# Optimization experiments

Measured on AMD Instinct MI355X. Metric: run time of the kernel, lower is better.

The kernel has to match this reference:

```python
import jax, jax.numpy as jnp
import numpy as np

HID = 64
NUM_LAYERS = 2
EPS = 1e-5


def _layernorm(x, g, b):
    mu = jnp.mean(x, axis=-1, keepdims=True)
    var = jnp.mean(jnp.square(x - mu), axis=-1, keepdims=True)
    return (x - mu) * jax.lax.rsqrt(var + EPS) * g + b


def _mlp(x, w1, b1, g, beta, w2, b2):
    # Linear -> LayerNorm -> ReLU -> Linear (torch Linear: x @ W.T + b)
    h = x @ w1.T + b1
    h = jax.nn.relu(_layernorm(h, g, beta))
    return h @ w2.T + b2


def _gru(x, h, wih, whh, bih, bhh):
    # PyTorch GRUCell semantics
    gi = x @ wih.T + bih
    gh = h @ whh.T + bhh
    ir, iz, inn = jnp.split(gi, 3, axis=-1)
    hr, hz, hn = jnp.split(gh, 3, axis=-1)
    r = jax.nn.sigmoid(ir + hr)
    z = jax.nn.sigmoid(iz + hz)
    n = jnp.tanh(inn + r * hn)
    return (1.0 - z) * n + z * h


def setup_inputs() -> dict:
    key = jax.random.key(0)
    ks = iter(jax.random.split(key, 64))
    s = 0.05

    def rn(shape):
        return jax.random.normal(next(ks), shape, dtype=jnp.float32) * s

    B, M, K1 = 32, 256, 128
    inp = {
        'hybrid_input': jax.random.normal(next(ks), (B, M, K1, 4), dtype=jnp.float32),
        'hidden_state': jnp.zeros((B, HID), dtype=jnp.float32),
        # input encoder
        'enc_w1': rn((HID, 4)), 'enc_b1': rn((HID,)),
        'enc_g': jnp.ones((HID,), jnp.float32), 'enc_beta': jnp.zeros((HID,), jnp.float32),
        'enc_w2': rn((HID, HID)), 'enc_b2': rn((HID,)),
        # per-layer, per-side (axis0=layer, axis1=[row,col]) params
        'l_w1': rn((NUM_LAYERS, 2, HID, HID)), 'l_b1': rn((NUM_LAYERS, 2, HID)),
        'l_g': jnp.ones((NUM_LAYERS, 2, HID), jnp.float32), 'l_beta': jnp.zeros((NUM_LAYERS, 2, HID), jnp.float32),
        'l_w2': rn((NUM_LAYERS, 2, HID, HID)), 'l_b2': rn((NUM_LAYERS, 2, HID)),
        'l_gwih': rn((NUM_LAYERS, 2, 3 * HID, HID)), 'l_gwhh': rn((NUM_LAYERS, 2, 3 * HID, HID)),
        'l_gbih': rn((NUM_LAYERS, 2, 3 * HID)), 'l_gbhh': rn((NUM_LAYERS, 2, 3 * HID)),
        # top-level GRU
        'g_wih': rn((3 * HID, HID)), 'g_whh': rn((3 * HID, HID)),
        'g_bih': rn((3 * HID,)), 'g_bhh': rn((3 * HID,)),
        # head: Linear(2H->H) -> ReLU -> Linear(H->1)
        'head_w1': rn((HID, 2 * HID)), 'head_b1': rn((HID,)),
        'head_w2': rn((1, HID)), 'head_b2': rn((1,)),
    }
    return inp


def reference(hybrid_input, hidden_state, enc_w1, enc_b1, enc_g, enc_beta, enc_w2, enc_b2,
              l_w1, l_b1, l_g, l_beta, l_w2, l_b2, l_gwih, l_gwhh, l_gbih, l_gbhh,
              g_wih, g_whh, g_bih, g_bhh, head_w1, head_b1, head_w2, head_b2):
    # input encoder
    x = _mlp(hybrid_input, enc_w1, enc_b1, enc_g, enc_beta, enc_w2, enc_b2)

    for l in range(NUM_LAYERS):
        # row pass: max over axis 2 (K+1)
        row_max = jnp.max(x, axis=2, keepdims=True)
        upd = _mlp(x - row_max, l_w1[l, 0], l_b1[l, 0], l_g[l, 0], l_beta[l, 0], l_w2[l, 0], l_b2[l, 0])
        x = _gru(upd, x, l_gwih[l, 0], l_gwhh[l, 0], l_gbih[l, 0], l_gbhh[l, 0])
        # col pass: max over axis 1 (M)
        col_max = jnp.max(x, axis=1, keepdims=True)
        upd = _mlp(x - col_max, l_w1[l, 1], l_b1[l, 1], l_g[l, 1], l_beta[l, 1], l_w2[l, 1], l_b2[l, 1])
        x = _gru(upd, x, l_gwih[l, 1], l_gwhh[l, 1], l_gbih[l, 1], l_gbhh[l, 1])

    B, M, K1, h = x.shape
    global_feat = jnp.max(x.reshape(B, M * K1, h), axis=1)  # (B, H)
    new_hidden = _gru(global_feat, hidden_state, g_wih, g_whh, g_bih, g_bhh)

    h_exp = jnp.broadcast_to(new_hidden[:, None, None, :], (B, M, K1, h))
    combined = jnp.concatenate([x, h_exp], axis=-1)  # (B, M, K1, 2H)
    hh = jax.nn.relu(combined @ head_w1.T + head_b1)
    logits = (hh @ head_w2.T + head_b2)[..., 0]  # (B, M, K1)
    return logits, new_hidden
```

## Files before the change

kernel.cpp:

```cpp
#include <hip/hip_runtime.h>
#include <math.h>

typedef unsigned int u32;
typedef unsigned short u16;
typedef __attribute__((ext_vector_type(4))) float f32x4;
typedef __attribute__((ext_vector_type(8))) short s16x8;

#define NTOT 1048576
#define SWZ(n, col) ((col) ^ (((n) & 7) << 4))

__device__ __forceinline__ u16 f2bf(float f) {
  u32 u = __float_as_uint(f);
  u32 r = ((u >> 16) & 1u) + 0x7fffu;
  return (u16)((u + r) >> 16);
}
__device__ __forceinline__ float bflo(u32 v) { return __uint_as_float(v << 16); }
__device__ __forceinline__ float bfhi(u32 v) { return __uint_as_float(v & 0xffff0000u); }
__device__ __forceinline__ u32 pk2(float a, float b) {
  return (u32)f2bf(a) | ((u32)f2bf(b) << 16);
}
__device__ __forceinline__ float sigm(float x) {
  return __builtin_amdgcn_rcpf(1.0f + __expf(-x));
}
__device__ __forceinline__ float tanh_f(float x) {
  float e = __expf(2.0f * x);
  return 1.0f - 2.0f * __builtin_amdgcn_rcpf(e + 1.0f);
}
__device__ __forceinline__ float relu(float x) { return fmaxf(x, 0.0f); }

__device__ __forceinline__ void gemm16(const unsigned char* L, int aoff, int boff,
                                       int w, int lq, int lr, f32x4 acc[4]) {
  const int l = lq * 16 + lr;
  s16x8 a0 = *(const s16x8*)(L + aoff + ((w * 2 + 0) * 64 + l) * 16);
  s16x8 a1 = *(const s16x8*)(L + aoff + ((w * 2 + 1) * 64 + l) * 16);
  const int c0 = ((lq << 4)) ^ ((lr & 7) << 4);
  const unsigned char* Bp = L + boff + lr * 128;
#pragma unroll
  for (int nt = 0; nt < 4; ++nt) {
    s16x8 b0 = *(const s16x8*)(Bp + nt * 2048 + c0);
    s16x8 b1 = *(const s16x8*)(Bp + nt * 2048 + (c0 ^ 64));
    acc[nt] = __builtin_amdgcn_mfma_f32_16x16x32_bf16(a0, b0, acc[nt], 0, 0, 0);
    acc[nt] = __builtin_amdgcn_mfma_f32_16x16x32_bf16(a1, b1, acc[nt], 0, 0, 0);
  }
}

__device__ __forceinline__ void binit(f32x4 acc[4], float x, float y, float z, float w) {
  f32x4 v; v[0] = x; v[1] = y; v[2] = z; v[3] = w;
#pragma unroll
  for (int nt = 0; nt < 4; ++nt) acc[nt] = v;
}

__global__ void diag_kernel(float* out, float v) { out[0] = v; }

__global__ __launch_bounds__(256) void prep_kernel(
    const float* __restrict__ enc_w2, const float* __restrict__ head_w1,
    const float* __restrict__ l_w1, const float* __restrict__ l_w2,
    const float* __restrict__ l_gwih, const float* __restrict__ l_gwhh,
    ushort* __restrict__ gwF) {
  const int id = blockIdx.x;
  const int t = threadIdx.x;
  const float* src;
  int ld = 64;
  if (id == 0)      { src = enc_w2; }
  else if (id == 1) { src = head_w1; ld = 128; }
  else if (id < 6)  { src = l_w1 + (id - 2) * 4096; }
  else if (id < 10) { src = l_w2 + (id - 6) * 4096; }
  else if (id < 22) { int q = id - 10; src = l_gwih + (q / 3) * 12288 + (q % 3) * 4096; }
  else              { int q = id - 22; src = l_gwhh + (q / 3) * 12288 + (q % 3) * 4096; }
  uint4* dst = (uint4*)(gwF + (size_t)id * 4096);
#pragma unroll
  for (int i = 0; i < 2; ++i) {
    int ch = i * 256 + t;
    int q = ch & 63;
    int g = ch >> 6;
    int j = (g >> 1) * 16 + (q & 15);
    int k = (g & 1) * 32 + (q >> 4) * 8;
    const float* s = src + (size_t)j * ld + k;
    float4 f0 = *(const float4*)(s);
    float4 f1 = *(const float4*)(s + 4);
    uint4 o;
    o.x = pk2(f0.x, f0.y); o.y = pk2(f0.z, f0.w);
    o.z = pk2(f1.x, f1.y); o.w = pk2(f1.z, f1.w);
    dst[ch] = o;
  }
}

__global__ __launch_bounds__(256) void encoder_kernel(
    const float4* __restrict__ hyb, ushort* __restrict__ xG,
    const ushort* __restrict__ gwF, const float* __restrict__ enc_w1,
    const float* __restrict__ b1, const float* __restrict__ gg,
    const float* __restrict__ be, const float* __restrict__ b2) {
  __shared__ __align__(16) unsigned char L[25600];
  const int t = threadIdx.x;
  const int w = t >> 6, l = t & 63, lq = l >> 4, lr = l & 15;
  const int gbase = blockIdx.x * 64;

  { const uint4* src = (const uint4*)gwF;
    *(uint4*)(L + 16384 + t * 16) = src[t];
    *(uint4*)(L + 16384 + (256 + t) * 16) = src[256 + t]; }
  ((float*)(L + 24576))[t] = enc_w1[t];
  __syncthreads();

  {
    const int n = t >> 2, part = t & 3;
    float4 iv = hyb[gbase + n];
    const float* W1 = (const float*)(L + 24576);
    float h[16];
#pragma unroll
    for (int jj = 0; jj < 16; ++jj) {
      int j = part * 16 + jj;
      float4 wr = *(const float4*)(W1 + j * 4);
      h[jj] = b1[j] + wr.x * iv.x + wr.y * iv.y + wr.z * iv.z + wr.w * iv.w;
    }
    float s = 0.f, q = 0.f;
#pragma unroll
    for (int jj = 0; jj < 16; ++jj) { s += h[jj]; q += h[jj] * h[jj]; }
    s += __shfl_xor(s, 1); q += __shfl_xor(q, 1);
    s += __shfl_xor(s, 2); q += __shfl_xor(q, 2);
    float mean = s * (1.f / 64.f);
    float rstd = rsqrtf(q * (1.f / 64.f) - mean * mean + 1e-5f);
    u32 pk[8];
#pragma unroll
    for (int jj = 0; jj < 16; jj += 2) {
      int j = part * 16 + jj;
      float v0 = relu((h[jj] - mean) * rstd * gg[j] + be[j]);
      float v1 = relu((h[jj + 1] - mean) * rstd * gg[j + 1] + be[j + 1]);
      pk[jj >> 1] = pk2(v0, v1);
    }
    *(uint4*)(L + n * 128 + SWZ(n, part * 32))      = make_uint4(pk[0], pk[1], pk[2], pk[3]);
    *(uint4*)(L + n * 128 + SWZ(n, part * 32 + 16)) = make_uint4(pk[4], pk[5], pk[6], pk[7]);
  }
  __syncthreads();

  const int j0 = w * 16 + lq * 4;
  float4 vb2 = *(const float4*)(b2 + j0);
  f32x4 acc[4];
  binit(acc, vb2.x, vb2.y, vb2.z, vb2.w);
  gemm16(L, 16384, 0, w, lq, lr, acc);
  const int colb = w * 32 + lq * 8;
#pragma unroll
  for (int nt = 0; nt < 4; ++nt) {
    int n = nt * 16 + lr;
    *(uint2*)(L + 8192 + n * 128 + SWZ(n, colb)) =
        make_uint2(pk2(acc[nt][0], acc[nt][1]), pk2(acc[nt][2], acc[nt][3]));
  }
  __syncthreads();
#pragma unroll
  for (int i = 0; i < 2; ++i) {
    int flat = i * 256 + t; int n = flat >> 3, c = flat & 7;
    uint4 v = *(const uint4*)(L + 8192 + n * 128 + SWZ(n, c * 16));
    ((uint4*)(xG + (size_t)gbase * 64))[(size_t)n * 8 + c] = v;
  }
}

#define LXL 0
#define LP  8192
#define LWB(i) (16384 + (i) * 8192)
#define LRED 49152

__global__ __launch_bounds__(256, 3) void pass_kernel(
    ushort* __restrict__ xG, const ushort* __restrict__ gwF,
    const float* __restrict__ rmG, const float* __restrict__ cmG, int mode,
    int s_w1, int s_w2, int s_ih0, int s_hh0,
    const float* __restrict__ b1, const float* __restrict__ b2,
    const float* __restrict__ gg, const float* __restrict__ be,
    const float* __restrict__ bih, const float* __restrict__ bhh) {
  __shared__ __align__(16) unsigned char L[51200];
  const int t = threadIdx.x;
  const int w = t >> 6, l = t & 63, lq = l >> 4, lr = l & 15;
  const int gbase = blockIdx.x * 64;
  const int j0 = w * 16 + lq * 4;
  const int colb = w * 32 + lq * 8;

  float4 vb1 = *(const float4*)(b1 + j0);
  float4 vg  = *(const float4*)(gg + j0);
  float4 vbe = *(const float4*)(be + j0);
  float4 vb2 = *(const float4*)(b2 + j0);
  float4 bi0 = *(const float4*)(bih + j0),       bh0 = *(const float4*)(bhh + j0);
  float4 bi1 = *(const float4*)(bih + 64 + j0),  bh1 = *(const float4*)(bhh + 64 + j0);
  float4 bi2 = *(const float4*)(bih + 128 + j0), bh2 = *(const float4*)(bhh + 128 + j0);

  {
    int sl[4] = {s_w1, s_w2, s_ih0, s_hh0};
#pragma unroll
    for (int sbi = 0; sbi < 4; ++sbi) {
      const uint4* src = (const uint4*)(gwF + (size_t)sl[sbi] * 4096);
      *(uint4*)(L + LWB(sbi) + t * 16) = src[t];
      *(uint4*)(L + LWB(sbi) + (256 + t) * 16) = src[256 + t];
    }
  }
  {
    const int rbase = (gbase >> 7) * 64;
    const int cbase = (gbase >> 15) * 128 + (gbase & 127);
    const uint4* xrow = (const uint4*)(xG + (size_t)gbase * 64);
#pragma unroll
    for (int i = 0; i < 2; ++i) {
      int flat = i * 256 + t; int n = flat >> 3, c = flat & 7;
      uint4 xv = xrow[(size_t)n * 8 + c];
      *(uint4*)(L + LXL + n * 128 + SWZ(n, c * 16)) = xv;
      const float* mvp = (mode == 0) ? (rmG + rbase + c * 8)
                                     : (cmG + (size_t)(cbase + n) * 64 + c * 8);
      float4 ma = *(const float4*)(mvp);
      float4 mb = *(const float4*)(mvp + 4);
      uint4 o;
      o.x = pk2(bflo(xv.x) - ma.x, bfhi(xv.x) - ma.y);
      o.y = pk2(bflo(xv.y) - ma.z, bfhi(xv.y) - ma.w);
      o.z = pk2(bflo(xv.z) - mb.x, bfhi(xv.z) - mb.y);
      o.w = pk2(bflo(xv.w) - mb.z, bfhi(xv.w) - mb.w);
      *(uint4*)(L + LP + n * 128 + SWZ(n, c * 16)) = o;
    }
  }
  __syncthreads();

  f32x4 acc[4];
  binit(acc, vb1.x, vb1.y, vb1.z, vb1.w);
  gemm16(L, LWB(0), LP, w, lq, lr, acc);
#pragma unroll
  for (int nt = 0; nt < 4; ++nt) {
    float s = acc[nt][0] + acc[nt][1] + acc[nt][2] + acc[nt][3];
    float q = acc[nt][0] * acc[nt][0] + acc[nt][1] * acc[nt][1] +
              acc[nt][2] * acc[nt][2] + acc[nt][3] * acc[nt][3];
    s += __shfl_xor(s, 16); q += __shfl_xor(q, 16);
    s += __shfl_xor(s, 32); q += __shfl_xor(q, 32);
    if (lq == 0) *(float2*)(L + LRED + (w * 64 + nt * 16 + lr) * 8) = make_float2(s, q);
  }
  __syncthreads();
  {
    const uint4* src = (const uint4*)(gwF + (size_t)(s_ih0 + 1) * 4096);
    *(uint4*)(L + LWB(0) + t * 16) = src[t];
    *(uint4*)(L + LWB(0) + (256 + t) * 16) = src[256 + t];
  }
  {
    float gv[4] = {vg.x, vg.y, vg.z, vg.w};
    float bv[4] = {vbe.x, vbe.y, vbe.z, vbe.w};
#pragma unroll
    for (int nt = 0; nt < 4; ++nt) {
      int n = nt * 16 + lr;
      float ss = 0.f, qq = 0.f;
#pragma unroll
      for (int wv = 0; wv < 4; ++wv) {
        float2 pr = *(const float2*)(L + LRED + (wv * 64 + n) * 8);
        ss += pr.x; qq += pr.y;
      }
      float mean = ss * (1.f / 64.f);
      float rstd = rsqrtf(qq * (1.f / 64.f) - mean * mean + 1e-5f);
      float h_[4];
#pragma unroll
      for (int r = 0; r < 4; ++r) h_[r] = relu((acc[nt][r] - mean) * rstd * gv[r] + bv[r]);
      *(uint2*)(L + LP + n * 128 + SWZ(n, colb)) =
          make_uint2(pk2(h_[0], h_[1]), pk2(h_[2], h_[3]));
    }
  }
  __syncthreads();

  binit(acc, vb2.x, vb2.y, vb2.z, vb2.w);
  gemm16(L, LWB(1), LP, w, lq, lr, acc);
  __syncthreads();
  {
    const uint4* src = (const uint4*)(gwF + (size_t)(s_hh0 + 1) * 4096);
    *(uint4*)(L + LWB(1) + t * 16) = src[t];
    *(uint4*)(L + LWB(1) + (256 + t) * 16) = src[256 + t];
  }
#pragma unroll
  for (int nt = 0; nt < 4; ++nt) {
    int n = nt * 16 + lr;
    *(uint2*)(L + LP + n * 128 + SWZ(n, colb)) =
        make_uint2(pk2(acc[nt][0], acc[nt][1]), pk2(acc[nt][2], acc[nt][3]));
  }
  __syncthreads();

  binit(acc, bi0.x + bh0.x, bi0.y + bh0.y, bi0.z + bh0.z, bi0.w + bh0.w);
  gemm16(L, LWB(2), LP, w, lq, lr, acc);
  gemm16(L, LWB(3), LXL, w, lq, lr, acc);
  float rg[4][4];
#pragma unroll
  for (int nt = 0; nt < 4; ++nt)
#pragma unroll
    for (int r = 0; r < 4; ++r) rg[nt][r] = sigm(acc[nt][r]);
  __syncthreads();
  {
    const uint4* s2 = (const uint4*)(gwF + (size_t)(s_ih0 + 2) * 4096);
    const uint4* s3 = (const uint4*)(gwF + (size_t)(s_hh0 + 2) * 4096);
    *(uint4*)(L + LWB(2) + t * 16) = s2[t];
    *(uint4*)(L + LWB(2) + (256 + t) * 16) = s2[256 + t];
    *(uint4*)(L + LWB(3) + t * 16) = s3[t];
    *(uint4*)(L + LWB(3) + (256 + t) * 16) = s3[256 + t];
  }
  binit(acc, bi1.x + bh1.x, bi1.y + bh1.y, bi1.z + bh1.z, bi1.w + bh1.w);
  gemm16(L, LWB(0), LP, w, lq, lr, acc);
  gemm16(L, LWB(1), LXL, w, lq, lr, acc);
  float zg[4][4];
#pragma unroll
  for (int nt = 0; nt < 4; ++nt)
#pragma unroll
    for (int r = 0; r < 4; ++r) zg[nt][r] = sigm(acc[nt][r]);
  __syncthreads();

  f32x4 ai[4], ah[4];
  binit(ai, bi2.x, bi2.y, bi2.z, bi2.w);
  gemm16(L, LWB(2), LP, w, lq, lr, ai);
  binit(ah, bh2.x, bh2.y, bh2.z, bh2.w);
  gemm16(L, LWB(3), LXL, w, lq, lr, ah);

  float xn[4][4];
#pragma unroll
  for (int nt = 0; nt < 4; ++nt) {
    int n = nt * 16 + lr;
    uint2 xo = *(const uint2*)(L + LXL + n * 128 + SWZ(n, colb));
    float xv[4] = {bflo(xo.x), bfhi(xo.x), bflo(xo.y), bfhi(xo.y)};
#pragma unroll
    for (int r = 0; r < 4; ++r) {
      float nn = tanh_f(ai[nt][r] + rg[nt][r] * ah[nt][r]);
      xn[nt][r] = (1.0f - zg[nt][r]) * nn + zg[nt][r] * xv[r];
    }
  }
  __syncthreads();
#pragma unroll
  for (int nt = 0; nt < 4; ++nt) {
    int n = nt * 16 + lr;
    *(uint2*)(L + LXL + n * 128 + SWZ(n, colb)) =
        make_uint2(pk2(xn[nt][0], xn[nt][1]), pk2(xn[nt][2], xn[nt][3]));
  }
  __syncthreads();
#pragma unroll
  for (int i = 0; i < 2; ++i) {
    int flat = i * 256 + t; int n = flat >> 3, c = flat & 7;
    uint4 v = *(const uint4*)(L + LXL + n * 128 + SWZ(n, c * 16));
    ((uint4*)(xG + (size_t)gbase * 64))[(size_t)n * 8 + c] = v;
  }
}

__global__ __launch_bounds__(256) void rowmax_kernel(const ushort* __restrict__ xG,
                                                     float* __restrict__ rm) {
  __shared__ float red[8][64];
  const int t = threadIdx.x;
  const int col = t & 31, rg = t >> 5;
  const u32* xu = (const u32*)xG + (size_t)blockIdx.x * 128 * 32;
  float m0 = -INFINITY, m1 = -INFINITY;
#pragma unroll 4
  for (int i = 0; i < 16; ++i) {
    u32 v = xu[(size_t)(rg + i * 8) * 32 + col];
    m0 = fmaxf(m0, bflo(v)); m1 = fmaxf(m1, bfhi(v));
  }
  red[rg][col * 2] = m0; red[rg][col * 2 + 1] = m1;
  __syncthreads();
  if (t < 64) {
    float m = red[0][t];
#pragma unroll
    for (int i = 1; i < 8; ++i) m = fmaxf(m, red[i][t]);
    rm[(size_t)blockIdx.x * 64 + t] = m;
  }
}

__global__ __launch_bounds__(256) void colmax_kernel(const ushort* __restrict__ xG,
                                                     float* __restrict__ cm) {
  const int t = threadIdx.x;
  const int b = blockIdx.x >> 4, kg = blockIdx.x & 15;
  const int col = t & 31, k1 = kg * 8 + (t >> 5);
  const u32* xu = (const u32*)xG;
  float m0 = -INFINITY, m1 = -INFINITY;
  for (int m = 0; m < 256; ++m) {
    size_t node = ((size_t)(b * 256 + m)) * 128 + k1;
    u32 v = xu[node * 32 + col];
    m0 = fmaxf(m0, bflo(v)); m1 = fmaxf(m1, bfhi(v));
  }
  float* dst = cm + ((size_t)(b * 128 + k1)) * 64 + col * 2;
  dst[0] = m0; dst[1] = m1;
}

__global__ __launch_bounds__(256) void gmax_kernel(const ushort* __restrict__ xG,
                                                   float* __restrict__ gp) {
  __shared__ float red[8][64];
  const int t = threadIdx.x;
  const int b = blockIdx.x >> 3, ng = blockIdx.x & 7;
  const int col = t & 31, rg = t >> 5;
  const u32* xu = (const u32*)xG + ((size_t)(b * 32768 + ng * 4096)) * 32;
  float m0 = -INFINITY, m1 = -INFINITY;
  for (int i = 0; i < 512; ++i) {
    u32 v = xu[(size_t)(rg + i * 8) * 32 + col];
    m0 = fmaxf(m0, bflo(v)); m1 = fmaxf(m1, bfhi(v));
  }
  red[rg][col * 2] = m0; red[rg][col * 2 + 1] = m1;
  __syncthreads();
  if (t < 64) {
    float m = red[0][t];
#pragma unroll
    for (int i = 1; i < 8; ++i) m = fmaxf(m, red[i][t]);
    gp[(size_t)blockIdx.x * 64 + t] = m;
  }
}

__global__ __launch_bounds__(64) void topgru_kernel(
    const float* __restrict__ gp, const float* __restrict__ hs,
    const float* __restrict__ gwih, const float* __restrict__ gwhh,
    const float* __restrict__ gbih, const float* __restrict__ gbhh,
    float* __restrict__ nh, float* __restrict__ outTail) {
  __shared__ float gf[64], h0[64];
  const int b = blockIdx.x, j = threadIdx.x;
  float gv = gp[b * 512 + j];
#pragma unroll
  for (int i = 1; i < 8; ++i) gv = fmaxf(gv, gp[b * 512 + i * 64 + j]);
  gf[j] = gv;
  h0[j] = hs[b * 64 + j];
  __syncthreads();
  float gi[3], gh[3];
#pragma unroll
  for (int g = 0; g < 3; ++g) {
    float s = gbih[g * 64 + j];
    const float* wr = gwih + (g * 64 + j) * 64;
    for (int k = 0; k < 64; ++k) s += wr[k] * gf[k];
    gi[g] = s;
  }
#pragma unroll
  for (int g = 0; g < 3; ++g) {
    float s = gbhh[g * 64 + j];
    const float* wr = gwhh + (g * 64 + j) * 64;
    for (int k = 0; k < 64; ++k) s += wr[k] * h0[k];
    gh[g] = s;
  }
  float rr = sigm(gi[0] + gh[0]);
  float zz = sigm(gi[1] + gh[1]);
  float nn = tanh_f(gi[2] + rr * gh[2]);
  float val = (1.0f - zz) * nn + zz * h0[j];
  nh[b * 64 + j] = val;
  outTail[b * 64 + j] = val;
}

__global__ __launch_bounds__(64) void hc_kernel(const float* __restrict__ nh,
                                                const float* __restrict__ hw1,
                                                const float* __restrict__ hb1,
                                                float* __restrict__ hc) {
  __shared__ float h0[64];
  const int b = blockIdx.x, j = threadIdx.x;
  h0[j] = nh[b * 64 + j];
  __syncthreads();
  float s = hb1[j];
  const float* wr = hw1 + j * 128 + 64;
  for (int k = 0; k < 64; ++k) s += wr[k] * h0[k];
  hc[b * 64 + j] = s;
}

__global__ __launch_bounds__(256) void head_kernel(
    const ushort* __restrict__ xG, const ushort* __restrict__ gwF,
    const float* __restrict__ hc, const float* __restrict__ hw2,
    const float* __restrict__ hb2, float* __restrict__ out) {
  __shared__ __align__(16) unsigned char L[17408];
  const int t = threadIdx.x;
  const int w = t >> 6, l = t & 63, lq = l >> 4, lr = l & 15;
  const int gbase = blockIdx.x * 64;
  const int b = gbase >> 15;
  const int j0 = w * 16 + lq * 4;

  { const uint4* src = (const uint4*)(gwF + 4096);
    *(uint4*)(L + 8192 + t * 16) = src[t];
    *(uint4*)(L + 8192 + (256 + t) * 16) = src[256 + t]; }
  { const uint4* xrow = (const uint4*)(xG + (size_t)gbase * 64);
#pragma unroll
    for (int i = 0; i < 2; ++i) {
      int flat = i * 256 + t; int n = flat >> 3, c = flat & 7;
      *(uint4*)(L + n * 128 + SWZ(n, c * 16)) = xrow[(size_t)n * 8 + c];
    } }
  __syncthreads();

  float4 vhc = *(const float4*)(hc + b * 64 + j0);
  f32x4 acc[4];
  binit(acc, vhc.x, vhc.y, vhc.z, vhc.w);
  gemm16(L, 8192, 0, w, lq, lr, acc);

  float4 w2v = *(const float4*)(hw2 + j0);
  float w2a[4] = {w2v.x, w2v.y, w2v.z, w2v.w};
#pragma unroll
  for (int nt = 0; nt < 4; ++nt) {
    float p = 0.f;
#pragma unroll
    for (int r = 0; r < 4; ++r) p += w2a[r] * relu(acc[nt][r]);
    p += __shfl_xor(p, 16);
    p += __shfl_xor(p, 32);
    if (lq == 0) ((float*)(L + 16384))[w * 64 + nt * 16 + lr] = p;
  }
  __syncthreads();
  if (t < 64) {
    const float* red = (const float*)(L + 16384);
    out[gbase + t] = red[t] + red[64 + t] + red[128 + t] + red[192 + t] + hb2[0];
  }
}

extern "C" void kernel_launch(void* const* d_in, const int* in_sizes, int n_in,
                              void* d_out, int out_size, void* d_ws, size_t ws_size,
                              hipStream_t stream) {
  const float* hybrid   = (const float*)d_in[0];
  const float* hidden   = (const float*)d_in[1];
  const float* enc_w1   = (const float*)d_in[2];
  const float* enc_b1   = (const float*)d_in[3];
  const float* enc_g    = (const float*)d_in[4];
  const float* enc_beta = (const float*)d_in[5];
  const float* enc_w2   = (const float*)d_in[6];
  const float* enc_b2   = (const float*)d_in[7];
  const float* l_w1     = (const float*)d_in[8];
  const float* l_b1     = (const float*)d_in[9];
  const float* l_g      = (const float*)d_in[10];
  const float* l_beta   = (const float*)d_in[11];
  const float* l_w2     = (const float*)d_in[12];
  const float* l_b2     = (const float*)d_in[13];
  const float* l_gwih   = (const float*)d_in[14];
  const float* l_gwhh   = (const float*)d_in[15];
  const float* l_gbih   = (const float*)d_in[16];
  const float* l_gbhh   = (const float*)d_in[17];
  const float* g_wih    = (const float*)d_in[18];
  const float* g_whh    = (const float*)d_in[19];
  const float* g_bih    = (const float*)d_in[20];
  const float* g_bhh    = (const float*)d_in[21];
  const float* head_w1  = (const float*)d_in[22];
  const float* head_b1  = (const float*)d_in[23];
  const float* head_w2  = (const float*)d_in[24];
  const float* head_b2  = (const float*)d_in[25];

  char* p = (char*)d_ws;
  size_t off = 0;
  auto carve = [&](size_t bytes) { void* r = p + off; off = (off + bytes + 255) & ~255ULL; return r; };
  ushort* xG  = (ushort*)carve((size_t)NTOT * 64 * 2);
  ushort* gwF = (ushort*)carve(34 * 4096 * 2);
  float*  rmG = (float*)carve(8192 * 64 * 4);
  float*  cmG = (float*)carve((size_t)32 * 128 * 64 * 4);
  float*  gp  = (float*)carve(256 * 64 * 4);
  float*  nh  = (float*)carve(2048 * 4);
  float*  hcb = (float*)carve(2048 * 4);

  if (ws_size < off) {
    diag_kernel<<<1, 1, 0, stream>>>((float*)d_out, 1.0f + (float)ws_size * 1e-9f);
    return;
  }

  prep_kernel<<<34, 256, 0, stream>>>(enc_w2, head_w1, l_w1, l_w2, l_gwih, l_gwhh, gwF);
  encoder_kernel<<<16384, 256, 0, stream>>>((const float4*)hybrid, xG, gwF, enc_w1,
                                            enc_b1, enc_g, enc_beta, enc_b2);

  for (int lyr = 0; lyr < 2; ++lyr) {
    for (int s = 0; s < 2; ++s) {
      const int m = lyr * 2 + s;
      if (s == 0) rowmax_kernel<<<8192, 256, 0, stream>>>(xG, rmG);
      else        colmax_kernel<<<512, 256, 0, stream>>>(xG, cmG);
      pass_kernel<<<16384, 256, 0, stream>>>(
          xG, gwF, rmG, cmG, s,
          2 + m, 6 + m, 10 + 3 * m, 22 + 3 * m,
          l_b1 + m * 64, l_b2 + m * 64, l_g + m * 64, l_beta + m * 64,
          l_gbih + m * 192, l_gbhh + m * 192);
    }
  }

  gmax_kernel<<<256, 256, 0, stream>>>(xG, gp);
  topgru_kernel<<<32, 64, 0, stream>>>(gp, hidden, g_wih, g_whh, g_bih, g_bhh,
                                       nh, (float*)d_out + 1048576);
  hc_kernel<<<32, 64, 0, stream>>>(nh, head_w1, head_b1, hcb);
  head_kernel<<<16384, 256, 0, stream>>>(xG, gwF, hcb, head_w2, head_b2, (float*)d_out);
}
```

Before: 878.2 us.

## Fuse row-max and global-max reductions into encoder and pass kernels

The encoder and pass kernels now compute the per-row max of their output in registers and LDS, and write it to the row-max buffer. This removes the separate rowmax kernels and the global-max kernel, each of which re-read the full activation tensor. The top-level GRU kernel now takes the global max over the per-row maxima. Blocks are widened to 512 threads covering 128 rows, so the weights staged per block serve twice as many rows, at the cost of more LDS per block and possibly lower occupancy. The fused row max is taken on fp32 values before bf16 rounding, so it can differ slightly from the max of the stored tensor.

```diff
diff --git a/kernel.cpp b/kernel.cpp
--- a/kernel.cpp
+++ b/kernel.cpp
@@ -9,13 +9,13 @@
 #define NTOT 1048576
 #define SWZ(n, col) ((col) ^ (((n) & 7) << 4))
 
+__device__ __forceinline__ float bflo(u32 v) { return __uint_as_float(v << 16); }
+__device__ __forceinline__ float bfhi(u32 v) { return __uint_as_float(v & 0xffff0000u); }
 __device__ __forceinline__ u16 f2bf(float f) {
   u32 u = __float_as_uint(f);
   u32 r = ((u >> 16) & 1u) + 0x7fffu;
   return (u16)((u + r) >> 16);
 }
-__device__ __forceinline__ float bflo(u32 v) { return __uint_as_float(v << 16); }
-__device__ __forceinline__ float bfhi(u32 v) { return __uint_as_float(v & 0xffff0000u); }
 __device__ __forceinline__ u32 pk2(float a, float b) {
   return (u32)f2bf(a) | ((u32)f2bf(b) << 16);
 }
@@ -31,10 +31,11 @@
 __device__ __forceinline__ void gemm16(const unsigned char* L, int aoff, int boff,
                                        int w, int lq, int lr, f32x4 acc[4]) {
   const int l = lq * 16 + lr;
-  s16x8 a0 = *(const s16x8*)(L + aoff + ((w * 2 + 0) * 64 + l) * 16);
-  s16x8 a1 = *(const s16x8*)(L + aoff + ((w * 2 + 1) * 64 + l) * 16);
-  const int c0 = ((lq << 4)) ^ ((lr & 7) << 4);
-  const unsigned char* Bp = L + boff + lr * 128;
+  const int ws = w & 3, nh = w >> 2;
+  s16x8 a0 = *(const s16x8*)(L + aoff + ((ws * 2 + 0) * 64 + l) * 16);
+  s16x8 a1 = *(const s16x8*)(L + aoff + ((ws * 2 + 1) * 64 + l) * 16);
+  const int c0 = (lq << 4) ^ ((lr & 7) << 4);
+  const unsigned char* Bp = L + boff + nh * 8192 + lr * 128;
 #pragma unroll
   for (int nt = 0; nt < 4; ++nt) {
     s16x8 b0 = *(const s16x8*)(Bp + nt * 2048 + c0);
@@ -85,26 +86,28 @@
   }
 }
 
-__global__ __launch_bounds__(256) void encoder_kernel(
+__global__ __launch_bounds__(512) void encoder_kernel(
     const float4* __restrict__ hyb, ushort* __restrict__ xG,
     const ushort* __restrict__ gwF, const float* __restrict__ enc_w1,
     const float* __restrict__ b1, const float* __restrict__ gg,
-    const float* __restrict__ be, const float* __restrict__ b2) {
-  __shared__ __align__(16) unsigned char L[25600];
+    const float* __restrict__ be, const float* __restrict__ b2,
+    float* __restrict__ rmOut) {
+  __shared__ __align__(16) unsigned char L[42496];
   const int t = threadIdx.x;
   const int w = t >> 6, l = t & 63, lq = l >> 4, lr = l & 15;
-  const int gbase = blockIdx.x * 64;
-
-  { const uint4* src = (const uint4*)gwF;
-    *(uint4*)(L + 16384 + t * 16) = src[t];
-    *(uint4*)(L + 16384 + (256 + t) * 16) = src[256 + t]; }
-  ((float*)(L + 24576))[t] = enc_w1[t];
+  const int ws = w & 3, nh = w >> 2;
+  const int gbase = blockIdx.x * 128;
+  const int j0 = ws * 16 + lq * 4;
+  const int colb = ws * 32 + lq * 8;
+
+  *(uint4*)(L + 32768 + t * 16) = ((const uint4*)gwF)[t];
+  if (t < 256) ((float*)(L + 40960))[t] = enc_w1[t];
   __syncthreads();
 
   {
     const int n = t >> 2, part = t & 3;
     float4 iv = hyb[gbase + n];
-    const float* W1 = (const float*)(L + 24576);
+    const float* W1 = (const float*)(L + 40960);
     float h[16];
 #pragma unroll
     for (int jj = 0; jj < 16; ++jj) {
@@ -132,45 +135,67 @@
   }
   __syncthreads();
 
-  const int j0 = w * 16 + lq * 4;
   float4 vb2 = *(const float4*)(b2 + j0);
   f32x4 acc[4];
   binit(acc, vb2.x, vb2.y, vb2.z, vb2.w);
-  gemm16(L, 16384, 0, w, lq, lr, acc);
-  const int colb = w * 32 + lq * 8;
-#pragma unroll
-  for (int nt = 0; nt < 4; ++nt) {
-    int n = nt * 16 + lr;
-    *(uint2*)(L + 8192 + n * 128 + SWZ(n, colb)) =
+  gemm16(L, 32768, 0, w, lq, lr, acc);
+#pragma unroll
+  for (int nt = 0; nt < 4; ++nt) {
+    int n = nh * 64 + nt * 16 + lr;
+    *(uint2*)(L + 16384 + n * 128 + SWZ(n, colb)) =
         make_uint2(pk2(acc[nt][0], acc[nt][1]), pk2(acc[nt][2], acc[nt][3]));
   }
-  __syncthreads();
-#pragma unroll
-  for (int i = 0; i < 2; ++i) {
-    int flat = i * 256 + t; int n = flat >> 3, c = flat & 7;
-    uint4 v = *(const uint4*)(L + 8192 + n * 128 + SWZ(n, c * 16));
-    ((uint4*)(xG + (size_t)gbase * 64))[(size_t)n * 8 + c] = v;
-  }
-}
-
-#define LXL 0
-#define LP  8192
-#define LWB(i) (16384 + (i) * 8192)
-#define LRED 49152
-
-__global__ __launch_bounds__(256, 3) void pass_kernel(
+  {
+    float mt[4];
+#pragma unroll
+    for (int r = 0; r < 4; ++r)
+      mt[r] = fmaxf(fmaxf(acc[0][r], acc[1][r]), fmaxf(acc[2][r], acc[3][r]));
+#pragma unroll
+    for (int m = 1; m < 16; m <<= 1)
+#pragma unroll
+      for (int r = 0; r < 4; ++r) mt[r] = fmaxf(mt[r], __shfl_xor(mt[r], m));
+    if (lr == 0) {
+      float4 v; v.x = mt[0]; v.y = mt[1]; v.z = mt[2]; v.w = mt[3];
+      *(float4*)(L + 41984 + (nh * 64 + j0) * 4) = v;
+    }
+  }
+  __syncthreads();
+  {
+    uint4* xout = (uint4*)(xG + (size_t)gbase * 64);
+#pragma unroll
+    for (int i = 0; i < 2; ++i) {
+      int flat = i * 512 + t; int n = flat >> 3, c = flat & 7;
+      xout[(size_t)n * 8 + c] = *(const uint4*)(L + 16384 + n * 128 + SWZ(n, c * 16));
+    }
+  }
+  if (t < 64) {
+    const float* R = (const float*)(L + 41984);
+    rmOut[(size_t)blockIdx.x * 64 + t] = fmaxf(R[t], R[64 + t]);
+  }
+}
+
+#define PXL 0
+#define PP  16384
+#define PWB(i) (32768 + (i) * 8192)
+#define PRED 65536
+
+__global__ __launch_bounds__(512, 4) void pass_kernel(
     ushort* __restrict__ xG, const ushort* __restrict__ gwF,
     const float* __restrict__ rmG, const float* __restrict__ cmG, int mode,
     int s_w1, int s_w2, int s_ih0, int s_hh0,
     const float* __restrict__ b1, const float* __restrict__ b2,
     const float* __restrict__ gg, const float* __restrict__ be,
-    const float* __restrict__ bih, const float* __restrict__ bhh) {
-  __shared__ __align__(16) unsigned char L[51200];
+    const float* __restrict__ bih, const float* __restrict__ bhh,
+    float* __restrict__ rmOut) {
+  __shared__ __align__(16) unsigned char L[69632];
   const int t = threadIdx.x;
   const int w = t >> 6, l = t & 63, lq = l >> 4, lr = l & 15;
-  const int gbase = blockIdx.x * 64;
-  const int j0 = w * 16 + lq * 4;
-  const int colb = w * 32 + lq * 8;
+  const int ws = w & 3, nh = w >> 2;
+  const int gbase = blockIdx.x * 128;
+  const int j0 = ws * 16 + lq * 4;
+  const int colb = ws * 32 + lq * 8;
+  const int row = blockIdx.x;
+  const int b = gbase >> 15;
 
   float4 vb1 = *(const float4*)(b1 + j0);
   float4 vg  = *(const float4*)(gg + j0);
@@ -183,23 +208,18 @@
   {
     int sl[4] = {s_w1, s_w2, s_ih0, s_hh0};
 #pragma unroll
-    for (int sbi = 0; sbi < 4; ++sbi) {
-      const uint4* src = (const uint4*)(gwF + (size_t)sl[sbi] * 4096);
-      *(uint4*)(L + LWB(sbi) + t * 16) = src[t];
-      *(uint4*)(L + LWB(sbi) + (256 + t) * 16) = src[256 + t];
-    }
-  }
-  {
-    const int rbase = (gbase >> 7) * 64;
-    const int cbase = (gbase >> 15) * 128 + (gbase & 127);
+    for (int sbi = 0; sbi < 4; ++sbi)
+      *(uint4*)(L + PWB(sbi) + t * 16) = ((const uint4*)(gwF + (size_t)sl[sbi] * 4096))[t];
+  }
+  {
     const uint4* xrow = (const uint4*)(xG + (size_t)gbase * 64);
 #pragma unroll
     for (int i = 0; i < 2; ++i) {
-      int flat = i * 256 + t; int n = flat >> 3, c = flat & 7;
+      int flat = i * 512 + t; int n = flat >> 3, c = flat & 7;
       uint4 xv = xrow[(size_t)n * 8 + c];
-      *(uint4*)(L + LXL + n * 128 + SWZ(n, c * 16)) = xv;
-      const float* mvp = (mode == 0) ? (rmG + rbase + c * 8)
-                                     : (cmG + (size_t)(cbase + n) * 64 + c * 8);
+      *(uint4*)(L + PXL + n * 128 + SWZ(n, c * 16)) = xv;
+      const float* mvp = (mode == 0) ? (rmG + (size_t)row * 64 + c * 8)
+                                     : (cmG + ((size_t)(b * 128 + n)) * 64 + c * 8);
       float4 ma = *(const float4*)(mvp);
       float4 mb = *(const float4*)(mvp + 4);
       uint4 o;
@@ -207,14 +227,14 @@
       o.y = pk2(bflo(xv.y) - ma.z, bfhi(xv.y) - ma.w);
       o.z = pk2(bflo(xv.z) - mb.x, bfhi(xv.z) - mb.y);
       o.w = pk2(bflo(xv.w) - mb.z, bfhi(xv.w) - mb.w);
-      *(uint4*)(L + LP + n * 128 + SWZ(n, c * 16)) = o;
+      *(uint4*)(L + PP + n * 128 + SWZ(n, c * 16)) = o;
     }
   }
   __syncthreads();
 
   f32x4 acc[4];
   binit(acc, vb1.x, vb1.y, vb1.z, vb1.w);
-  gemm16(L, LWB(0), LP, w, lq, lr, acc);
+  gemm16(L, PWB(0), PP, w, lq, lr, acc);
 #pragma unroll
   for (int nt = 0; nt < 4; ++nt) {
     float s = acc[nt][0] + acc[nt][1] + acc[nt][2] + acc[nt][3];
@@ -222,24 +242,23 @@
               acc[nt][2] * acc[nt][2] + acc[nt][3] * acc[nt][3];
     s += __shfl_xor(s, 16); q += __shfl_xor(q, 16);
     s += __shfl_xor(s, 32); q += __shfl_xor(q, 32);
-    if (lq == 0) *(float2*)(L + LRED + (w * 64 + nt * 16 + lr) * 8) = make_float2(s, q);
-  }
-  __syncthreads();
-  {
-    const uint4* src = (const uint4*)(gwF + (size_t)(s_ih0 + 1) * 4096);
-    *(uint4*)(L + LWB(0) + t * 16) = src[t];
-    *(uint4*)(L + LWB(0) + (256 + t) * 16) = src[256 + t];
+    if (lq == 0)
+      *(float2*)(L + PRED + ((nh * 4 + ws) * 64 + nt * 16 + lr) * 8) = make_float2(s, q);
+  }
+  __syncthreads();
+  {
+    *(uint4*)(L + PWB(0) + t * 16) = ((const uint4*)(gwF + (size_t)(s_ih0 + 1) * 4096))[t];
   }
   {
     float gv[4] = {vg.x, vg.y, vg.z, vg.w};
     float bv[4] = {vbe.x, vbe.y, vbe.z, vbe.w};
 #pragma unroll
     for (int nt = 0; nt < 4; ++nt) {
-      int n = nt * 16 + lr;
+      int np = nt * 16 + lr;
       float ss = 0.f, qq = 0.f;
 #pragma unroll
       for (int wv = 0; wv < 4; ++wv) {
-        float2 pr = *(const float2*)(L + LRED + (wv * 64 + n) * 8);
+        float2 pr = *(const float2*)(L + PRED + ((nh * 4 + wv) * 64 + np) * 8);
         ss += pr.x; qq += pr.y;
       }
       float mean = ss * (1.f / 64.f);
@@ -247,31 +266,30 @@
       float h_[4];
 #pragma unroll
       for (int r = 0; r < 4; ++r) h_[r] = relu((acc[nt][r] - mean) * rstd * gv[r] + bv[r]);
-      *(uint2*)(L + LP + n * 128 + SWZ(n, colb)) =
+      int n = nh * 64 + np;
+      *(uint2*)(L + PP + n * 128 + SWZ(n, colb)) =
           make_uint2(pk2(h_[0], h_[1]), pk2(h_[2], h_[3]));
     }
   }
   __syncthreads();
 
   binit(acc, vb2.x, vb2.y, vb2.z, vb2.w);
-  gemm16(L, LWB(1), LP, w, lq, lr, acc);
-  __syncthreads();
-  {
-    const uint4* src = (const uint4*)(gwF + (size_t)(s_hh0 + 1) * 4096);
-    *(uint4*)(L + LWB(1) + t * 16) = src[t];
-    *(uint4*)(L + LWB(1) + (256 + t) * 16) = src[256 + t];
-  }
-#pragma unroll
-  for (int nt = 0; nt < 4; ++nt) {
-    int n = nt * 16 + lr;
-    *(uint2*)(L + LP + n * 128 + SWZ(n, colb)) =
+  gemm16(L, PWB(1), PP, w, lq, lr, acc);
+  __syncthreads();
+  {
+    *(uint4*)(L + PWB(1) + t * 16) = ((const uint4*)(gwF + (size_t)(s_hh0 + 1) * 4096))[t];
+  }
+#pragma unroll
+  for (int nt = 0; nt < 4; ++nt) {
+    int n = nh * 64 + nt * 16 + lr;
+    *(uint2*)(L + PP + n * 128 + SWZ(n, colb)) =
         make_uint2(pk2(acc[nt][0], acc[nt][1]), pk2(acc[nt][2], acc[nt][3]));
   }
   __syncthreads();
 
   binit(acc, bi0.x + bh0.x, bi0.y + bh0.y, bi0.z + bh0.z, bi0.w + bh0.w);
-  gemm16(L, LWB(2), LP, w, lq, lr, acc);
-  gemm16(L, LWB(3), LXL, w, lq, lr, acc);
+  gemm16(L, PWB(2), PP, w, lq, lr, acc);
+  gemm16(L, PWB(3), PXL, w, lq, lr, acc);
   float rg[4][4];
 #pragma unroll
   for (int nt = 0; nt < 4; ++nt)
@@ -279,16 +297,12 @@
     for (int r = 0; r < 4; ++r) rg[nt][r] = sigm(acc[nt][r]);
   __syncthreads();
   {
-    const uint4* s2 = (const uint4*)(gwF + (size_t)(s_ih0 + 2) * 4096);
-    const uint4* s3 = (const uint4*)(gwF + (size_t)(s_hh0 + 2) * 4096);
-    *(uint4*)(L + LWB(2) + t * 16) = s2[t];
-    *(uint4*)(L + LWB(2) + (256 + t) * 16) = s2[256 + t];
-    *(uint4*)(L + LWB(3) + t * 16) = s3[t];
-    *(uint4*)(L + LWB(3) + (256 + t) * 16) = s3[256 + t];
+    *(uint4*)(L + PWB(2) + t * 16) = ((const uint4*)(gwF + (size_t)(s_ih0 + 2) * 4096))[t];
+    *(uint4*)(L + PWB(3) + t * 16) = ((const uint4*)(gwF + (size_t)(s_hh0 + 2) * 4096))[t];
   }
   binit(acc, bi1.x + bh1.x, bi1.y + bh1.y, bi1.z + bh1.z, bi1.w + bh1.w);
-  gemm16(L, LWB(0), LP, w, lq, lr, acc);
-  gemm16(L, LWB(1), LXL, w, lq, lr, acc);
+  gemm16(L, PWB(0), PP, w, lq, lr, acc);
+  gemm16(L, PWB(1), PXL, w, lq, lr, acc);
   float zg[4][4];
 #pragma unroll
   for (int nt = 0; nt < 4; ++nt)
@@ -298,57 +312,55 @@
 
   f32x4 ai[4], ah[4];
   binit(ai, bi2.x, bi2.y, bi2.z, bi2.w);
-  gemm16(L, LWB(2), LP, w, lq, lr, ai);
+  gemm16(L, PWB(2), PP, w, lq, lr, ai);
   binit(ah, bh2.x, bh2.y, bh2.z, bh2.w);
-  gemm16(L, LWB(3), LXL, w, lq, lr, ah);
+  gemm16(L, PWB(3), PXL, w, lq, lr, ah);
 
   float xn[4][4];
 #pragma unroll
   for (int nt = 0; nt < 4; ++nt) {
-    int n = nt * 16 + lr;
-    uint2 xo = *(const uint2*)(L + LXL + n * 128 + SWZ(n, colb));
+    int n = nh * 64 + nt * 16 + lr;
+    uint2 xo = *(const uint2*)(L + PXL + n * 128 + SWZ(n, colb));
     float xv[4] = {bflo(xo.x), bfhi(xo.x), bflo(xo.y), bfhi(xo.y)};
 #pragma unroll
     for (int r = 0; r < 4; ++r) {
       float nn = tanh_f(ai[nt][r] + rg[nt][r] * ah[nt][r]);
-      xn[nt][r] = (1.0f - zg[nt][r]) * nn + zg[nt][r] * xv[r];
-    }
-  }
-  __syncthreads();
-#pragma unroll
-  for (int nt = 0; nt < 4; ++nt) {
-    int n = nt * 16 + lr;
-    *(uint2*)(L + LXL + n * 128 + SWZ(n, colb)) =
+      xn[nt][r] = nn + zg[nt][r] * (xv[r] - nn);
+    }
+  }
+  __syncthreads();
+#pragma unroll
+  for (int nt = 0; nt < 4; ++nt) {
+    int n = nh * 64 + nt * 16 + lr;
+    *(uint2*)(L + PXL + n * 128 + SWZ(n, colb)) =
         make_uint2(pk2(xn[nt][0], xn[nt][1]), pk2(xn[nt][2], xn[nt][3]));
   }
-  __syncthreads();
-#pragma unroll
-  for (int i = 0; i < 2; ++i) {
-    int flat = i * 256 + t; int n = flat >> 3, c = flat & 7;
-    uint4 v = *(const uint4*)(L + LXL + n * 128 + SWZ(n, c * 16));
-    ((uint4*)(xG + (size_t)gbase * 64))[(size_t)n * 8 + c] = v;
-  }
-}
-
-__global__ __launch_bounds__(256) void rowmax_kernel(const ushort* __restrict__ xG,
-                                                     float* __restrict__ rm) {
-  __shared__ float red[8][64];
-  const int t = threadIdx.x;
-  const int col = t & 31, rg = t >> 5;
-  const u32* xu = (const u32*)xG + (size_t)blockIdx.x * 128 * 32;
-  float m0 = -INFINITY, m1 = -INFINITY;
-#pragma unroll 4
-  for (int i = 0; i < 16; ++i) {
-    u32 v = xu[(size_t)(rg + i * 8) * 32 + col];
-    m0 = fmaxf(m0, bflo(v)); m1 = fmaxf(m1, bfhi(v));
-  }
-  red[rg][col * 2] = m0; red[rg][col * 2 + 1] = m1;
-  __syncthreads();
+  {
+    float mt[4];
+#pragma unroll
+    for (int r = 0; r < 4; ++r)
+      mt[r] = fmaxf(fmaxf(xn[0][r], xn[1][r]), fmaxf(xn[2][r], xn[3][r]));
+#pragma unroll
+    for (int m = 1; m < 16; m <<= 1)
+#pragma unroll
+      for (int r = 0; r < 4; ++r) mt[r] = fmaxf(mt[r], __shfl_xor(mt[r], m));
+    if (lr == 0) {
+      float4 v; v.x = mt[0]; v.y = mt[1]; v.z = mt[2]; v.w = mt[3];
+      *(float4*)(L + PRED + (nh * 64 + j0) * 4) = v;
+    }
+  }
+  __syncthreads();
+  {
+    uint4* xout = (uint4*)(xG + (size_t)gbase * 64);
+#pragma unroll
+    for (int i = 0; i < 2; ++i) {
+      int flat = i * 512 + t; int n = flat >> 3, c = flat & 7;
+      xout[(size_t)n * 8 + c] = *(const uint4*)(L + PXL + n * 128 + SWZ(n, c * 16));
+    }
+  }
   if (t < 64) {
-    float m = red[0][t];
-#pragma unroll
-    for (int i = 1; i < 8; ++i) m = fmaxf(m, red[i][t]);
-    rm[(size_t)blockIdx.x * 64 + t] = m;
+    const float* R = (const float*)(L + PRED);
+    rmOut[(size_t)row * 64 + t] = fmaxf(R[t], R[64 + t]);
   }
 }
 
@@ -368,39 +380,22 @@
   dst[0] = m0; dst[1] = m1;
 }
 
-__global__ __launch_bounds__(256) void gmax_kernel(const ushort* __restrict__ xG,
-                                                   float* __restrict__ gp) {
-  __shared__ float red[8][64];
-  const int t = threadIdx.x;
-  const int b = blockIdx.x >> 3, ng = blockIdx.x & 7;
-  const int col = t & 31, rg = t >> 5;
-  const u32* xu = (const u32*)xG + ((size_t)(b * 32768 + ng * 4096)) * 32;
-  float m0 = -INFINITY, m1 = -INFINITY;
-  for (int i = 0; i < 512; ++i) {
-    u32 v = xu[(size_t)(rg + i * 8) * 32 + col];
-    m0 = fmaxf(m0, bflo(v)); m1 = fmaxf(m1, bfhi(v));
-  }
-  red[rg][col * 2] = m0; red[rg][col * 2 + 1] = m1;
-  __syncthreads();
-  if (t < 64) {
-    float m = red[0][t];
-#pragma unroll
-    for (int i = 1; i < 8; ++i) m = fmaxf(m, red[i][t]);
-    gp[(size_t)blockIdx.x * 64 + t] = m;
-  }
-}
-
 __global__ __launch_bounds__(64) void topgru_kernel(
-    const float* __restrict__ gp, const float* __restrict__ hs,
+    const float* __restrict__ rm, const float* __restrict__ hs,
     const float* __restrict__ gwih, const float* __restrict__ gwhh,
     const float* __restrict__ gbih, const float* __restrict__ gbhh,
     float* __restrict__ nh, float* __restrict__ outTail) {
   __shared__ float gf[64], h0[64];
   const int b = blockIdx.x, j = threadIdx.x;
-  float gv = gp[b * 512 + j];
-#pragma unroll
-  for (int i = 1; i < 8; ++i) gv = fmaxf(gv, gp[b * 512 + i * 64 + j]);
-  gf[j] = gv;
+  float g0 = -INFINITY, g1 = -INFINITY, g2 = -INFINITY, g3 = -INFINITY;
+  const float* base = rm + (size_t)b * 256 * 64 + j;
+  for (int r = 0; r < 256; r += 4) {
+    g0 = fmaxf(g0, base[(r + 0) * 64]);
+    g1 = fmaxf(g1, base[(r + 1) * 64]);
+    g2 = fmaxf(g2, base[(r + 2) * 64]);
+    g3 = fmaxf(g3, base[(r + 3) * 64]);
+  }
+  gf[j] = fmaxf(fmaxf(g0, g1), fmaxf(g2, g3));
   h0[j] = hs[b * 64 + j];
   __syncthreads();
   float gi[3], gh[3];
@@ -520,9 +515,8 @@
   auto carve = [&](size_t bytes) { void* r = p + off; off = (off + bytes + 255) & ~255ULL; return r; };
   ushort* xG  = (ushort*)carve((size_t)NTOT * 64 * 2);
   ushort* gwF = (ushort*)carve(34 * 4096 * 2);
-  float*  rmG = (float*)carve(8192 * 64 * 4);
+  float*  rmG = (float*)carve((size_t)8192 * 64 * 4);
   float*  cmG = (float*)carve((size_t)32 * 128 * 64 * 4);
-  float*  gp  = (float*)carve(256 * 64 * 4);
   float*  nh  = (float*)carve(2048 * 4);
   float*  hcb = (float*)carve(2048 * 4);
 
@@ -532,24 +526,22 @@
   }
 
   prep_kernel<<<34, 256, 0, stream>>>(enc_w2, head_w1, l_w1, l_w2, l_gwih, l_gwhh, gwF);
-  encoder_kernel<<<16384, 256, 0, stream>>>((const float4*)hybrid, xG, gwF, enc_w1,
-                                            enc_b1, enc_g, enc_beta, enc_b2);
+  encoder_kernel<<<8192, 512, 0, stream>>>((const float4*)hybrid, xG, gwF, enc_w1,
+                                           enc_b1, enc_g, enc_beta, enc_b2, rmG);
 
   for (int lyr = 0; lyr < 2; ++lyr) {
     for (int s = 0; s < 2; ++s) {
       const int m = lyr * 2 + s;
-      if (s == 0) rowmax_kernel<<<8192, 256, 0, stream>>>(xG, rmG);
-      else        colmax_kernel<<<512, 256, 0, stream>>>(xG, cmG);
-      pass_kernel<<<16384, 256, 0, stream>>>(
+      if (s == 1) colmax_kernel<<<512, 256, 0, stream>>>(xG, cmG);
+      pass_kernel<<<8192, 512, 0, stream>>>(
           xG, gwF, rmG, cmG, s,
           2 + m, 6 + m, 10 + 3 * m, 22 + 3 * m,
           l_b1 + m * 64, l_b2 + m * 64, l_g + m * 64, l_beta + m * 64,
-          l_gbih + m * 192, l_gbhh + m * 192);
-    }
-  }
-
-  gmax_kernel<<<256, 256, 0, stream>>>(xG, gp);
-  topgru_kernel<<<32, 64, 0, stream>>>(gp, hidden, g_wih, g_whh, g_bih, g_bhh,
+          l_gbih + m * 192, l_gbhh + m * 192, rmG);
+    }
+  }
+
+  topgru_kernel<<<32, 64, 0, stream>>>(rmG, hidden, g_wih, g_whh, g_bih, g_bhh,
                                        nh, (float*)d_out + 1048576);
   hc_kernel<<<32, 64, 0, stream>>>(nh, head_w1, head_b1, hcb);
   head_kernel<<<16384, 256, 0, stream>>>(xG, gwF, hcb, head_w2, head_b2, (float*)d_out);
```

Result: faster. 814.2 us (-7.3%).
